# Performance work log

Measured on AMD Instinct MI355X. Metric: run time of the kernel, lower is better.

## Reference

```python
import jax, jax.numpy as jnp
import numpy as np

B, T, H = 4, 2048, 1024
NH = 16
DK = H // NH  # 64
EPS = 1e-12


def setup_inputs() -> dict:
    key = jax.random.key(0)
    ks = jax.random.split(key, 20)
    s = 0.02
    inp = {
        "hidden_states": jax.random.normal(ks[0], (B, T, H), jnp.float32),
        "source_states": jax.random.normal(ks[1], (B, T, H), jnp.float32),
        "source_len": jax.random.randint(ks[2], (B,), 0, T, jnp.int64),
        # attention params (Linear: y = x @ W + b)
        "Wq": s * jax.random.normal(ks[3], (H, H), jnp.float32),
        "bq": jnp.zeros((H,), jnp.float32),
        "Wk": s * jax.random.normal(ks[4], (H, H), jnp.float32),
        "bk": jnp.zeros((H,), jnp.float32),
        "Wv": s * jax.random.normal(ks[5], (H, H), jnp.float32),
        "bv": jnp.zeros((H,), jnp.float32),
        "Wd": s * jax.random.normal(ks[6], (H, H), jnp.float32),
        "bd": jnp.zeros((H,), jnp.float32),
        # Fp: Linear -> ReLU -> (dropout, eval=id) -> Linear -> (dropout)
        "Wp1": s * jax.random.normal(ks[7], (H, H), jnp.float32),
        "bp1": jnp.zeros((H,), jnp.float32),
        "Wp2": s * jax.random.normal(ks[8], (H, H), jnp.float32),
        "bp2": jnp.zeros((H,), jnp.float32),
        # LayerNorm
        "ln_g": jnp.ones((H,), jnp.float32),
        "ln_b": jnp.zeros((H,), jnp.float32),
    }
    return inp


def _split_heads(x):
    # (B, T, H) -> (B, NH, T, DK)
    return x.reshape(B, T, NH, DK).transpose(0, 2, 1, 3)


def reference(hidden_states, source_states, source_len, Wq, bq, Wk, bk, Wv, bv,
              Wd, bd, Wp1, bp1, Wp2, bp2, ln_g, ln_b):
    # P = Fp(source_states), masked to valid source positions
    P = jax.nn.relu(source_states @ Wp1 + bp1) @ Wp2 + bp2  # (B,T,H)
    rng = jnp.arange(T)[None, :]                              # (1,T)
    source_mask = rng < source_len[:, None]                   # (B,T) bool
    P = P * source_mask[:, :, None].astype(P.dtype)

    q = _split_heads(hidden_states @ Wq + bq)  # (B,NH,T,DK)
    k = _split_heads(P @ Wk + bk)
    v = _split_heads(P @ Wv + bv)

    scores = jnp.einsum('bhqd,bhkd->bhqk', q, k) / jnp.sqrt(jnp.float32(DK))
    scores = scores + (1.0 - source_mask[:, None, None, :].astype(scores.dtype)) * -10000.0
    probs = jax.nn.softmax(scores.astype(jnp.float32), axis=-1).astype(hidden_states.dtype)

    ctx = jnp.einsum('bhqk,bhkd->bhqd', probs, v)            # (B,NH,T,DK)
    ctx = ctx.transpose(0, 2, 1, 3).reshape(B, T, H)

    attn_out = ctx @ Wd + bd
    x = attn_out + hidden_states
    mu = jnp.mean(x, axis=-1, keepdims=True)
    var = jnp.mean(jnp.square(x - mu), axis=-1, keepdims=True)
    out = (x - mu) * jax.lax.rsqrt(var + EPS) * ln_g + ln_b
    return out
```

## Files before the change

### kernel.cpp

```cpp
#include <hip/hip_runtime.h>
#include <hip/hip_bf16.h>

#define BB 4
#define TT 2048
#define HH 1024
#define NHH 16
#define DKK 64

typedef __attribute__((ext_vector_type(8))) short bf16x8;
typedef __attribute__((ext_vector_type(4))) float f32x4;

__device__ __forceinline__ unsigned short f2bf(float f) {
    union { float f; unsigned u; } v; v.f = f;
    unsigned r = v.u + 0x7fffu + ((v.u >> 16) & 1u);
    return (unsigned short)(r >> 16);
}

__device__ __forceinline__ void gload_lds16(const unsigned short* g, unsigned short* l) {
    __builtin_amdgcn_global_load_lds(
        (const __attribute__((address_space(1))) unsigned int*)g,
        (__attribute__((address_space(3))) unsigned int*)l, 16, 0, 0);
}

__global__ __launch_bounds__(256) void cvt_kernel(const float* __restrict__ in,
                                                  unsigned short* __restrict__ out, int n4) {
    int i = blockIdx.x * blockDim.x + threadIdx.x;
    if (i < n4) {
        float4 v = reinterpret_cast<const float4*>(in)[i];
        union { unsigned short u[4]; unsigned long long ll; } o;
        o.u[0] = f2bf(v.x); o.u[1] = f2bf(v.y); o.u[2] = f2bf(v.z); o.u[3] = f2bf(v.w);
        reinterpret_cast<unsigned long long*>(out)[i] = o.ll;
    }
}

__global__ __launch_bounds__(256) void wtcvt_kernel(const float* __restrict__ W,
                                                    unsigned short* __restrict__ Wt) {
    __shared__ float t[32][33];
    int bx = blockIdx.x * 32, by = blockIdx.y * 32;
    int tx = threadIdx.x, ty = threadIdx.y;
#pragma unroll
    for (int i = 0; i < 32; i += 8)
        t[ty + i][tx] = W[(size_t)(by + ty + i) * HH + bx + tx];
    __syncthreads();
#pragma unroll
    for (int i = 0; i < 32; i += 8)
        Wt[(size_t)(bx + ty + i) * HH + by + tx] = f2bf(t[tx][ty + i]);
}

template <int EPI, bool SKIP>
__global__ __launch_bounds__(256) void gemm_kernel(
    const unsigned short* __restrict__ A, const unsigned short* __restrict__ Bt,
    const float* __restrict__ bias, unsigned short* __restrict__ Cb,
    float* __restrict__ Cf, const float* __restrict__ resid,
    const int* __restrict__ slen, int M, int N, int K) {
    __shared__ unsigned short As[128 * 64];
    __shared__ unsigned short Bs[128 * 64];
    int by = blockIdx.y * 128, bx = blockIdx.x * 128;
    if constexpr (SKIP) {
        int slb = slen[by >> 11];
        int ktend = ((slb + 63) >> 6) << 6;
        if (ktend == 0) ktend = 64;
        if ((by & (TT - 1)) >= ktend) return;
    }
    int tid = threadIdx.x, lane = tid & 63, w = tid >> 6;
    int wr = (w >> 1) * 64, wc = (w & 1) * 64;

    f32x4 acc[4][4] = {};
    for (int k0 = 0; k0 < K; k0 += 64) {
        __syncthreads();
#pragma unroll
        for (int c = 0; c < 4; c++) {
            int idx = c * 256 + tid;
            int r = idx >> 3, col = (idx & 7) * 8;
            gload_lds16(&A[(size_t)(by + r) * K + k0 + col], &As[idx * 8]);
            gload_lds16(&Bt[(size_t)(bx + r) * K + k0 + col], &Bs[idx * 8]);
        }
        __syncthreads();
#pragma unroll
        for (int kk = 0; kk < 2; kk++) {
            bf16x8 a[4], b[4];
#pragma unroll
            for (int i = 0; i < 4; i++)
                a[i] = *(bf16x8*)&As[(wr + i * 16 + (lane & 15)) * 64 + kk * 32 + (lane >> 4) * 8];
#pragma unroll
            for (int j = 0; j < 4; j++)
                b[j] = *(bf16x8*)&Bs[(wc + j * 16 + (lane & 15)) * 64 + kk * 32 + (lane >> 4) * 8];
#pragma unroll
            for (int i = 0; i < 4; i++)
#pragma unroll
                for (int j = 0; j < 4; j++)
                    acc[i][j] = __builtin_amdgcn_mfma_f32_16x16x32_bf16(a[i], b[j], acc[i][j], 0, 0, 0);
        }
    }

    int sl = 0;
    if constexpr (EPI == 2) sl = slen[by >> 11];
#pragma unroll
    for (int i = 0; i < 4; i++)
#pragma unroll
        for (int j = 0; j < 4; j++)
#pragma unroll
            for (int r = 0; r < 4; r++) {
                int row = by + wr + i * 16 + (lane >> 4) * 4 + r;
                int col = bx + wc + j * 16 + (lane & 15);
                float v = acc[i][j][r] + bias[col];
                if constexpr (EPI == 1) v = fmaxf(v, 0.f);
                if constexpr (EPI == 2) { int t = row & (TT - 1); if (t >= sl) v = 0.f; }
                if constexpr (EPI == 1 || EPI == 2) {
                    Cb[(size_t)row * N + col] = f2bf(v);
                } else if constexpr (EPI == 3) {
                    int b = row >> 11, t = row & (TT - 1), h = col >> 6, d = col & 63;
                    Cb[((size_t)((b * NHH + h) * TT + t)) * DKK + d] = f2bf(v);
                } else if constexpr (EPI == 4) {
                    int b = row >> 11, t = row & (TT - 1), h = col >> 6, d = col & 63;
                    Cb[((size_t)((b * NHH + h) * DKK + d)) * TT + t] = f2bf(v);
                } else if constexpr (EPI == 5) {
                    Cf[(size_t)row * N + col] = v + resid[(size_t)row * N + col];
                }
            }
}

__global__ __launch_bounds__(256) void attn_kernel(
    const unsigned short* __restrict__ Q, const unsigned short* __restrict__ K,
    const unsigned short* __restrict__ Vt, const int* __restrict__ slen,
    unsigned short* __restrict__ ctx) {
    __shared__ unsigned short Ks[64 * 72];
    __shared__ unsigned short Vs[64 * 72];
    __shared__ unsigned short Pl[4][16 * 64];
    int tid = threadIdx.x, lane = tid & 63, w = tid >> 6;
    int c = lane & 15, g = lane >> 4;
    int b = blockIdx.z, h = blockIdx.y, q0 = blockIdx.x * 64;
    size_t bh = (size_t)(b * NHH + h);
    int sl = slen[b];
    int ktend = ((sl + 63) >> 6) << 6;
    if (ktend == 0) ktend = 64;

    bf16x8 qf[2];
    int qrow = q0 + w * 16 + c;
#pragma unroll
    for (int half = 0; half < 2; half++)
        qf[half] = *(const bf16x8*)&Q[(bh * TT + qrow) * DKK + half * 32 + g * 8];

    char* Pw = (char*)&Pl[w][0];
    unsigned swz = (unsigned)((c & 7) << 4);

    float m_ = -INFINITY, l_ = 0.f;
    f32x4 o[4] = {};

    for (int kt = 0; kt < ktend; kt += 64) {
        __syncthreads();
#pragma unroll
        for (int cc = 0; cc < 2; cc++) {
            int idx = tid + cc * 256;
            int r = idx >> 3, kc = (idx & 7) * 8;
            *(bf16x8*)&Ks[r * 72 + kc] = *(const bf16x8*)&K[(bh * TT + kt + r) * DKK + kc];
            *(bf16x8*)&Vs[r * 72 + kc] = *(const bf16x8*)&Vt[(bh * DKK + r) * TT + kt + kc];
        }
        __syncthreads();

        f32x4 s[4] = {};
        __builtin_amdgcn_s_setprio(1);
#pragma unroll
        for (int j = 0; j < 4; j++)
#pragma unroll
            for (int half = 0; half < 2; half++) {
                bf16x8 kf = *(bf16x8*)&Ks[(j * 16 + c) * 72 + half * 32 + g * 8];
                s[j] = __builtin_amdgcn_mfma_f32_16x16x32_bf16(kf, qf[half], s[j], 0, 0, 0);
            }
        __builtin_amdgcn_s_setprio(0);

        float sv[4][4];
#pragma unroll
        for (int j = 0; j < 4; j++) {
            int kbase = kt + j * 16 + g * 4;
#pragma unroll
            for (int r = 0; r < 4; r++)
                sv[j][r] = s[j][r] * 0.125f + ((kbase + r < sl) ? 0.f : -10000.f);
        }
        float tmax = -INFINITY;
#pragma unroll
        for (int j = 0; j < 4; j++)
#pragma unroll
            for (int r = 0; r < 4; r++) tmax = fmaxf(tmax, sv[j][r]);
        tmax = fmaxf(tmax, __shfl_xor(tmax, 16));
        tmax = fmaxf(tmax, __shfl_xor(tmax, 32));

        float mn = fmaxf(m_, tmax);
        float alpha = __expf(m_ - mn);
        float ps = 0.f;
#pragma unroll
        for (int j = 0; j < 4; j++)
#pragma unroll
            for (int r = 0; r < 4; r++) {
                float p = __expf(sv[j][r] - mn);
                sv[j][r] = p;
                ps += p;
            }
        ps += __shfl_xor(ps, 16);
        ps += __shfl_xor(ps, 32);
        l_ = l_ * alpha + ps;
        m_ = mn;

        float av[4];
#pragma unroll
        for (int r = 0; r < 4; r++) av[r] = __shfl(alpha, g * 4 + r);
#pragma unroll
        for (int go = 0; go < 4; go++)
#pragma unroll
            for (int r = 0; r < 4; r++) o[go][r] *= av[r];

#pragma unroll
        for (int j = 0; j < 4; j++) {
            __hip_bfloat162 lo = __float22bfloat162_rn(make_float2(sv[j][0], sv[j][1]));
            __hip_bfloat162 hi = __float22bfloat162_rn(make_float2(sv[j][2], sv[j][3]));
            uint2 u;
            u.x = *(unsigned*)&lo;
            u.y = *(unsigned*)&hi;
            *(uint2*)(Pw + c * 128 + (((unsigned)(j * 32 + g * 8)) ^ swz)) = u;
        }
        bf16x8 pf0 = *(bf16x8*)(Pw + c * 128 + (((unsigned)(g * 16)) ^ swz));
        bf16x8 pf1 = *(bf16x8*)(Pw + c * 128 + (((unsigned)(64 + g * 16)) ^ swz));

        __builtin_amdgcn_s_setprio(1);
#pragma unroll
        for (int go = 0; go < 4; go++) {
            bf16x8 vf0 = *(bf16x8*)&Vs[(go * 16 + c) * 72 + g * 8];
            o[go] = __builtin_amdgcn_mfma_f32_16x16x32_bf16(pf0, vf0, o[go], 0, 0, 0);
            bf16x8 vf1 = *(bf16x8*)&Vs[(go * 16 + c) * 72 + 32 + g * 8];
            o[go] = __builtin_amdgcn_mfma_f32_16x16x32_bf16(pf1, vf1, o[go], 0, 0, 0);
        }
        __builtin_amdgcn_s_setprio(0);
    }

    float linv[4];
#pragma unroll
    for (int r = 0; r < 4; r++) linv[r] = 1.f / __shfl(l_, g * 4 + r);
#pragma unroll
    for (int go = 0; go < 4; go++)
#pragma unroll
        for (int r = 0; r < 4; r++) {
            int t = q0 + w * 16 + g * 4 + r;
            int col = h * DKK + go * 16 + c;
            ctx[((size_t)(b * TT + t)) * HH + col] = f2bf(o[go][r] * linv[r]);
        }
}

__global__ __launch_bounds__(256) void ln_kernel(float* __restrict__ x,
                                                 const float* __restrict__ gam,
                                                 const float* __restrict__ bet) {
    int row = blockIdx.x, tid = threadIdx.x;
    float4 v = reinterpret_cast<float4*>(x)[(size_t)row * 256 + tid];
    float s = v.x + v.y + v.z + v.w;
#pragma unroll
    for (int m = 1; m < 64; m <<= 1) s += __shfl_xor(s, m);
    __shared__ float red[4], red2[4];
    if ((tid & 63) == 0) red[tid >> 6] = s;
    __syncthreads();
    float mean = (red[0] + red[1] + red[2] + red[3]) * (1.f / 1024.f);
    float dx0 = v.x - mean, dx1 = v.y - mean, dx2 = v.z - mean, dx3 = v.w - mean;
    float ss = dx0 * dx0 + dx1 * dx1 + dx2 * dx2 + dx3 * dx3;
#pragma unroll
    for (int m = 1; m < 64; m <<= 1) ss += __shfl_xor(ss, m);
    if ((tid & 63) == 0) red2[tid >> 6] = ss;
    __syncthreads();
    float var = (red2[0] + red2[1] + red2[2] + red2[3]) * (1.f / 1024.f);
    float rs = rsqrtf(var + 1e-12f);
    int c = tid * 4;
    float4 ov;
    ov.x = dx0 * rs * gam[c + 0] + bet[c + 0];
    ov.y = dx1 * rs * gam[c + 1] + bet[c + 1];
    ov.z = dx2 * rs * gam[c + 2] + bet[c + 2];
    ov.w = dx3 * rs * gam[c + 3] + bet[c + 3];
    reinterpret_cast<float4*>(x)[(size_t)row * 256 + tid] = ov;
}

extern "C" void kernel_launch(void* const* d_in, const int* in_sizes, int n_in,
                              void* d_out, int out_size, void* d_ws, size_t ws_size,
                              hipStream_t stream) {
    const float* hid  = (const float*)d_in[0];
    const float* src  = (const float*)d_in[1];
    const int* slen   = (const int*)d_in[2];
    const float* Wq  = (const float*)d_in[3];  const float* bq  = (const float*)d_in[4];
    const float* Wk  = (const float*)d_in[5];  const float* bk  = (const float*)d_in[6];
    const float* Wv  = (const float*)d_in[7];  const float* bv  = (const float*)d_in[8];
    const float* Wd  = (const float*)d_in[9];  const float* bd  = (const float*)d_in[10];
    const float* Wp1 = (const float*)d_in[11]; const float* bp1 = (const float*)d_in[12];
    const float* Wp2 = (const float*)d_in[13]; const float* bp2 = (const float*)d_in[14];
    const float* lng = (const float*)d_in[15]; const float* lnb = (const float*)d_in[16];

    char* ws = (char*)d_ws;
    const size_t MB = 1ull << 20;
    unsigned short* Wqt  = (unsigned short*)(ws + 0 * MB);
    unsigned short* Wkt  = (unsigned short*)(ws + 2 * MB);
    unsigned short* Wvt  = (unsigned short*)(ws + 4 * MB);
    unsigned short* Wdt  = (unsigned short*)(ws + 6 * MB);
    unsigned short* Wp1t = (unsigned short*)(ws + 8 * MB);
    unsigned short* Wp2t = (unsigned short*)(ws + 10 * MB);
    unsigned short* hidb = (unsigned short*)(ws + 12 * MB);
    unsigned short* srcb = (unsigned short*)(ws + 28 * MB);
    unsigned short* Ptmp = (unsigned short*)(ws + 44 * MB);
    unsigned short* Pb   = (unsigned short*)(ws + 60 * MB);
    unsigned short* Qb   = (unsigned short*)(ws + 76 * MB);
    unsigned short* Kb   = hidb;
    unsigned short* Vtb  = Ptmp;
    unsigned short* ctxb = srcb;

    dim3 tb(32, 8);
    wtcvt_kernel<<<dim3(32, 32), tb, 0, stream>>>(Wq, Wqt);
    wtcvt_kernel<<<dim3(32, 32), tb, 0, stream>>>(Wk, Wkt);
    wtcvt_kernel<<<dim3(32, 32), tb, 0, stream>>>(Wv, Wvt);
    wtcvt_kernel<<<dim3(32, 32), tb, 0, stream>>>(Wd, Wdt);
    wtcvt_kernel<<<dim3(32, 32), tb, 0, stream>>>(Wp1, Wp1t);
    wtcvt_kernel<<<dim3(32, 32), tb, 0, stream>>>(Wp2, Wp2t);

    const int n4 = (BB * TT * HH) / 4;
    cvt_kernel<<<n4 / 256, 256, 0, stream>>>(hid, hidb, n4);
    cvt_kernel<<<n4 / 256, 256, 0, stream>>>(src, srcb, n4);

    dim3 gg(HH / 128, (BB * TT) / 128);
    gemm_kernel<1, true><<<gg, 256, 0, stream>>>(srcb, Wp1t, bp1, Ptmp, nullptr, nullptr, slen, BB * TT, HH, HH);
    gemm_kernel<2, true><<<gg, 256, 0, stream>>>(Ptmp, Wp2t, bp2, Pb, nullptr, nullptr, slen, BB * TT, HH, HH);
    gemm_kernel<3, false><<<gg, 256, 0, stream>>>(hidb, Wqt, bq, Qb, nullptr, nullptr, slen, BB * TT, HH, HH);
    gemm_kernel<3, true><<<gg, 256, 0, stream>>>(Pb, Wkt, bk, Kb, nullptr, nullptr, slen, BB * TT, HH, HH);
    gemm_kernel<4, true><<<gg, 256, 0, stream>>>(Pb, Wvt, bv, Vtb, nullptr, nullptr, slen, BB * TT, HH, HH);
    attn_kernel<<<dim3(TT / 64, NHH, BB), 256, 0, stream>>>(Qb, Kb, Vtb, slen, ctxb);
    gemm_kernel<5, false><<<gg, 256, 0, stream>>>(ctxb, Wdt, bd, nullptr, (float*)d_out, hid, slen, BB * TT, HH, HH);
    ln_kernel<<<BB * TT, 256, 0, stream>>>((float*)d_out, lng, lnb);
}
```

Baseline: 305.3 us.

## Fold softmax scale into Q, use exp2 with lazy rescale, larger attention blocks

The Q projection epilogue now multiplies by 0.125*log2(e), so attention can use exp2 directly without a per-score scale. Masking is applied only on the tail tile. The running max and output rescale are skipped when the new tile max stays within a threshold of the old one. Attention blocks grow to 512 threads covering 128 queries, and K/V tiles load via global_load_lds into XOR-swizzled LDS without padding. This cuts softmax ALU work and halves K/V reloads per query, at the cost of bf16 rounding of a pre-scaled Q and exponent headroom from the lazy rescale.

```diff
diff --git a/kernel.cpp b/kernel.cpp
--- a/kernel.cpp
+++ b/kernel.cpp
@@ -106,9 +106,10 @@
                 float v = acc[i][j][r] + bias[col];
                 if constexpr (EPI == 1) v = fmaxf(v, 0.f);
                 if constexpr (EPI == 2) { int t = row & (TT - 1); if (t >= sl) v = 0.f; }
+                if constexpr (EPI == 6) v *= 0.18033688f;
                 if constexpr (EPI == 1 || EPI == 2) {
                     Cb[(size_t)row * N + col] = f2bf(v);
-                } else if constexpr (EPI == 3) {
+                } else if constexpr (EPI == 3 || EPI == 6) {
                     int b = row >> 11, t = row & (TT - 1), h = col >> 6, d = col & 63;
                     Cb[((size_t)((b * NHH + h) * TT + t)) * DKK + d] = f2bf(v);
                 } else if constexpr (EPI == 4) {
@@ -120,16 +121,16 @@
             }
 }
 
-__global__ __launch_bounds__(256) void attn_kernel(
+__global__ __launch_bounds__(512) void attn_kernel(
     const unsigned short* __restrict__ Q, const unsigned short* __restrict__ K,
     const unsigned short* __restrict__ Vt, const int* __restrict__ slen,
     unsigned short* __restrict__ ctx) {
-    __shared__ unsigned short Ks[64 * 72];
-    __shared__ unsigned short Vs[64 * 72];
-    __shared__ unsigned short Pl[4][16 * 64];
+    __shared__ unsigned short Ks[64 * 64];
+    __shared__ unsigned short Vs[64 * 64];
+    __shared__ unsigned short Pl[8][16 * 64];
     int tid = threadIdx.x, lane = tid & 63, w = tid >> 6;
     int c = lane & 15, g = lane >> 4;
-    int b = blockIdx.z, h = blockIdx.y, q0 = blockIdx.x * 64;
+    int b = blockIdx.z, h = blockIdx.y, q0 = blockIdx.x * 128;
     size_t bh = (size_t)(b * NHH + h);
     int sl = slen[b];
     int ktend = ((sl + 63) >> 6) << 6;
@@ -144,18 +145,16 @@
     char* Pw = (char*)&Pl[w][0];
     unsigned swz = (unsigned)((c & 7) << 4);
 
+    int sr = tid >> 3, ss = tid & 7;
+    int scol = (ss ^ (sr & 7)) * 8;
+
     float m_ = -INFINITY, l_ = 0.f;
     f32x4 o[4] = {};
 
     for (int kt = 0; kt < ktend; kt += 64) {
         __syncthreads();
-#pragma unroll
-        for (int cc = 0; cc < 2; cc++) {
-            int idx = tid + cc * 256;
-            int r = idx >> 3, kc = (idx & 7) * 8;
-            *(bf16x8*)&Ks[r * 72 + kc] = *(const bf16x8*)&K[(bh * TT + kt + r) * DKK + kc];
-            *(bf16x8*)&Vs[r * 72 + kc] = *(const bf16x8*)&Vt[(bh * DKK + r) * TT + kt + kc];
-        }
+        gload_lds16(&K[(bh * TT + kt + sr) * DKK + scol], &Ks[tid * 8]);
+        gload_lds16(&Vt[(bh * DKK + sr) * TT + kt + scol], &Vs[tid * 8]);
         __syncthreads();
 
         f32x4 s[4] = {};
@@ -164,55 +163,70 @@
         for (int j = 0; j < 4; j++)
 #pragma unroll
             for (int half = 0; half < 2; half++) {
-                bf16x8 kf = *(bf16x8*)&Ks[(j * 16 + c) * 72 + half * 32 + g * 8];
+                bf16x8 kf = *(bf16x8*)((char*)Ks + (j * 16 + c) * 128 +
+                                       (((unsigned)(half * 64 + g * 16)) ^ swz));
                 s[j] = __builtin_amdgcn_mfma_f32_16x16x32_bf16(kf, qf[half], s[j], 0, 0, 0);
             }
         __builtin_amdgcn_s_setprio(0);
 
-        float sv[4][4];
-#pragma unroll
-        for (int j = 0; j < 4; j++) {
-            int kbase = kt + j * 16 + g * 4;
-#pragma unroll
-            for (int r = 0; r < 4; r++)
-                sv[j][r] = s[j][r] * 0.125f + ((kbase + r < sl) ? 0.f : -10000.f);
-        }
+        if (kt + 64 > sl) {
+#pragma unroll
+            for (int j = 0; j < 4; j++) {
+                int kbase = kt + j * 16 + g * 4;
+#pragma unroll
+                for (int r = 0; r < 4; r++)
+                    if (kbase + r >= sl) s[j][r] = -14427.0f;
+            }
+        }
+
         float tmax = -INFINITY;
 #pragma unroll
         for (int j = 0; j < 4; j++)
 #pragma unroll
-            for (int r = 0; r < 4; r++) tmax = fmaxf(tmax, sv[j][r]);
+            for (int r = 0; r < 4; r++) tmax = fmaxf(tmax, s[j][r]);
         tmax = fmaxf(tmax, __shfl_xor(tmax, 16));
         tmax = fmaxf(tmax, __shfl_xor(tmax, 32));
 
-        float mn = fmaxf(m_, tmax);
-        float alpha = __expf(m_ - mn);
+        float p[4][4];
         float ps = 0.f;
-#pragma unroll
-        for (int j = 0; j < 4; j++)
-#pragma unroll
-            for (int r = 0; r < 4; r++) {
-                float p = __expf(sv[j][r] - mn);
-                sv[j][r] = p;
-                ps += p;
-            }
-        ps += __shfl_xor(ps, 16);
-        ps += __shfl_xor(ps, 32);
-        l_ = l_ * alpha + ps;
-        m_ = mn;
-
-        float av[4];
-#pragma unroll
-        for (int r = 0; r < 4; r++) av[r] = __shfl(alpha, g * 4 + r);
-#pragma unroll
-        for (int go = 0; go < 4; go++)
-#pragma unroll
-            for (int r = 0; r < 4; r++) o[go][r] *= av[r];
+        if (__all(tmax <= m_ + 8.f)) {
+#pragma unroll
+            for (int j = 0; j < 4; j++)
+#pragma unroll
+                for (int r = 0; r < 4; r++) {
+                    p[j][r] = __builtin_amdgcn_exp2f(s[j][r] - m_);
+                    ps += p[j][r];
+                }
+            ps += __shfl_xor(ps, 16);
+            ps += __shfl_xor(ps, 32);
+            l_ += ps;
+        } else {
+            float mn = fmaxf(m_, tmax);
+            float alpha = __builtin_amdgcn_exp2f(m_ - mn);
+#pragma unroll
+            for (int j = 0; j < 4; j++)
+#pragma unroll
+                for (int r = 0; r < 4; r++) {
+                    p[j][r] = __builtin_amdgcn_exp2f(s[j][r] - mn);
+                    ps += p[j][r];
+                }
+            ps += __shfl_xor(ps, 16);
+            ps += __shfl_xor(ps, 32);
+            l_ = l_ * alpha + ps;
+            m_ = mn;
+            float av[4];
+#pragma unroll
+            for (int r = 0; r < 4; r++) av[r] = __shfl(alpha, g * 4 + r);
+#pragma unroll
+            for (int go = 0; go < 4; go++)
+#pragma unroll
+                for (int r = 0; r < 4; r++) o[go][r] *= av[r];
+        }
 
 #pragma unroll
         for (int j = 0; j < 4; j++) {
-            __hip_bfloat162 lo = __float22bfloat162_rn(make_float2(sv[j][0], sv[j][1]));
-            __hip_bfloat162 hi = __float22bfloat162_rn(make_float2(sv[j][2], sv[j][3]));
+            __hip_bfloat162 lo = __float22bfloat162_rn(make_float2(p[j][0], p[j][1]));
+            __hip_bfloat162 hi = __float22bfloat162_rn(make_float2(p[j][2], p[j][3]));
             uint2 u;
             u.x = *(unsigned*)&lo;
             u.y = *(unsigned*)&hi;
@@ -224,9 +238,11 @@
         __builtin_amdgcn_s_setprio(1);
 #pragma unroll
         for (int go = 0; go < 4; go++) {
-            bf16x8 vf0 = *(bf16x8*)&Vs[(go * 16 + c) * 72 + g * 8];
+            bf16x8 vf0 = *(bf16x8*)((char*)Vs + (go * 16 + c) * 128 +
+                                    (((unsigned)(g * 16)) ^ swz));
             o[go] = __builtin_amdgcn_mfma_f32_16x16x32_bf16(pf0, vf0, o[go], 0, 0, 0);
-            bf16x8 vf1 = *(bf16x8*)&Vs[(go * 16 + c) * 72 + 32 + g * 8];
+            bf16x8 vf1 = *(bf16x8*)((char*)Vs + (go * 16 + c) * 128 +
+                                    (((unsigned)(64 + g * 16)) ^ swz));
             o[go] = __builtin_amdgcn_mfma_f32_16x16x32_bf16(pf1, vf1, o[go], 0, 0, 0);
         }
         __builtin_amdgcn_s_setprio(0);
@@ -320,10 +336,10 @@
     dim3 gg(HH / 128, (BB * TT) / 128);
     gemm_kernel<1, true><<<gg, 256, 0, stream>>>(srcb, Wp1t, bp1, Ptmp, nullptr, nullptr, slen, BB * TT, HH, HH);
     gemm_kernel<2, true><<<gg, 256, 0, stream>>>(Ptmp, Wp2t, bp2, Pb, nullptr, nullptr, slen, BB * TT, HH, HH);
-    gemm_kernel<3, false><<<gg, 256, 0, stream>>>(hidb, Wqt, bq, Qb, nullptr, nullptr, slen, BB * TT, HH, HH);
+    gemm_kernel<6, false><<<gg, 256, 0, stream>>>(hidb, Wqt, bq, Qb, nullptr, nullptr, slen, BB * TT, HH, HH);
     gemm_kernel<3, true><<<gg, 256, 0, stream>>>(Pb, Wkt, bk, Kb, nullptr, nullptr, slen, BB * TT, HH, HH);
     gemm_kernel<4, true><<<gg, 256, 0, stream>>>(Pb, Wvt, bv, Vtb, nullptr, nullptr, slen, BB * TT, HH, HH);
-    attn_kernel<<<dim3(TT / 64, NHH, BB), 256, 0, stream>>>(Qb, Kb, Vtb, slen, ctxb);
+    attn_kernel<<<dim3(TT / 128, NHH, BB), 512, 0, stream>>>(Qb, Kb, Vtb, slen, ctxb);
     gemm_kernel<5, false><<<gg, 256, 0, stream>>>(ctxb, Wdt, bd, nullptr, (float*)d_out, hid, slen, BB * TT, HH, HH);
     ln_kernel<<<BB * TT, 256, 0, stream>>>((float*)d_out, lng, lnb);
 }
```

Result: faster. 286.1 us (-6.3%).
